# Optimization experiments

Hardware: AMD Instinct MI355X
Metric: run time of the kernel (lower is better)

The kernel has to match this reference:

```python
import jax, jax.numpy as jnp
import numpy as np

C = 3.0              # Poincare ball curvature (hard-coded in module)
SQRT_C = np.float32(np.sqrt(3.0))
MIN_NORM = 1e-15     # geoopt MIN_NORM clamp
EPS = 1e-5           # artanh clamp for fp32
TEMP = 0.07


def setup_inputs() -> dict:
    key = jax.random.key(0)
    ks = jax.random.split(key, 6)
    B, F_IN, H, D, N = 4096, 768, 256, 128, 16384
    x = jax.random.normal(ks[0], (B, F_IN), jnp.float32)
    W1 = jax.random.normal(ks[1], (F_IN, H), jnp.float32) * np.float32(1.0 / np.sqrt(F_IN))
    b1 = jnp.zeros((H,), jnp.float32)
    W2 = jax.random.normal(ks[2], (H, H), jnp.float32) * np.float32(1.0 / np.sqrt(H))
    b2 = jnp.zeros((H,), jnp.float32)
    W3 = jax.random.normal(ks[3], (H, D), jnp.float32) * np.float32(1.0 / np.sqrt(H))
    b3 = jnp.zeros((D,), jnp.float32)
    # prototypes: unit directions scaled by 0.95/c (as in __init__), inside radius 1/sqrt(c)
    g = jax.random.normal(ks[4], (N, D), jnp.float32)
    prototypes = g / jnp.linalg.norm(g, axis=1, keepdims=True) * np.float32(0.95 / C)
    return {"x": x, "W1": W1, "b1": b1, "W2": W2, "b2": b2,
            "W3": W3, "b3": b3, "prototypes": prototypes}


def _expmap0(u):
    # geoopt expmap0: tanh(sqrt(c)*||u||) * u / (sqrt(c)*||u||)
    un = jnp.maximum(jnp.linalg.norm(u, axis=-1, keepdims=True), MIN_NORM)
    return jnp.tanh(SQRT_C * un) * u / (SQRT_C * un)


def _pairwise_poincare_dist(p, h):
    # dist(x,y) = 2/sqrt(c) * artanh( sqrt(c) * || (-x) mobius_add y || )
    # Expanded via dot products so no [B,N,D] intermediate is materialized.
    A = jnp.sum(p * p, axis=-1)            # [N]  ||p||^2
    Bn = jnp.sum(h * h, axis=-1)           # [B]  ||h||^2
    P = h @ p.T                            # [B,N] <h, p>
    # mobius_add(-p, h): <-p, h> = -P
    alpha = 1.0 - 2.0 * C * P + C * Bn[:, None]
    beta = 1.0 - C * A[None, :]
    denom = jnp.maximum(1.0 - 2.0 * C * P + (C * C) * A[None, :] * Bn[:, None], MIN_NORM)
    num_sq = alpha * alpha * A[None, :] + beta * beta * Bn[:, None] - 2.0 * alpha * beta * P
    mnorm = jnp.sqrt(jnp.maximum(num_sq, MIN_NORM)) / denom   # [B,N]
    arg = jnp.minimum(SQRT_C * mnorm, 1.0 - EPS)
    return (2.0 / SQRT_C) * jnp.arctanh(arg)                  # [B,N]


def reference(x, W1, b1, W2, b2, W3, b3, prototypes):
    # Mlp: Linear -> GELU -> Linear -> GELU -> Linear (exact erf GELU, torch default)
    h = jax.nn.gelu(x @ W1 + b1, approximate=False)
    h = jax.nn.gelu(h @ W2 + b2, approximate=False)
    u = h @ W3 + b3                       # [B, D] Euclidean embedding
    hyp = _expmap0(u)                     # [B, D] on Poincare ball
    dist = _pairwise_poincare_dist(prototypes, hyp)  # [B, N]
    logits = -dist / TEMP
    return logits, hyp
```

## Files before the change

kernel.cpp:

```cpp
#include <hip/hip_runtime.h>
#include <math.h>

#define BB 4096
#define FIN 768
#define HH 256
#define DD 128
#define NN 16384

typedef _Float16 half8 __attribute__((ext_vector_type(8)));
typedef _Float16 half4 __attribute__((ext_vector_type(4)));
typedef float floatx4 __attribute__((ext_vector_type(4)));

__global__ void transpose_kernel(const float* __restrict__ in, float* __restrict__ out,
                                 int K, int N) {
  __shared__ float tile[32][33];
  int k0 = blockIdx.y * 32, n0 = blockIdx.x * 32;
  int tx = threadIdx.x, ty = threadIdx.y;
  for (int r = ty; r < 32; r += 8) {
    tile[r][tx] = in[(size_t)(k0 + r) * N + (n0 + tx)];
  }
  __syncthreads();
  for (int r = ty; r < 32; r += 8) {
    out[(size_t)(n0 + r) * K + (k0 + tx)] = tile[tx][r];
  }
}

__global__ void proto_norms(const float* __restrict__ p, float* __restrict__ An) {
  int row = blockIdx.x * 4 + (threadIdx.x >> 6);
  int lane = threadIdx.x & 63;
  float v0 = p[(size_t)row * DD + lane], v1 = p[(size_t)row * DD + 64 + lane];
  float s = v0 * v0 + v1 * v1;
  for (int off = 32; off; off >>= 1) s += __shfl_xor(s, off);
  if (lane == 0) An[row] = s;
}

__global__ void expmap_kernel(const float* __restrict__ u, float* __restrict__ hyp,
                              float* __restrict__ sB) {
  int row = blockIdx.x * 4 + (threadIdx.x >> 6);
  int lane = threadIdx.x & 63;
  float u0 = u[(size_t)row * DD + lane], u1 = u[(size_t)row * DD + 64 + lane];
  double s = (double)u0 * u0 + (double)u1 * u1;
  for (int off = 32; off; off >>= 1) s += __shfl_xor(s, off);
  double un = sqrt(s);
  if (un < 1e-15) un = 1e-15;
  double t = 1.7320508075688772 * un;
  double factor = tanh(t) / t;
  float h0 = (float)(factor * u0), h1 = (float)(factor * u1);
  hyp[(size_t)row * DD + lane] = h0;
  hyp[(size_t)row * DD + 64 + lane] = h1;
  double bs = (double)h0 * h0 + (double)h1 * h1;
  for (int off = 32; off; off >>= 1) bs += __shfl_xor(bs, off);
  if (lane == 0) sB[row] = (float)(1.0 - 3.0 * bs);
}

template <int ACT>
__global__ __launch_bounds__(256) void gemm64(const float* __restrict__ A,
                                              const float* __restrict__ Bt,
                                              const float* __restrict__ bias,
                                              float* __restrict__ C,
                                              int M, int N, int K) {
  __shared__ __align__(16) float As[64 * 128];
  __shared__ __align__(16) float Bs[64 * 128];
  const int tx = threadIdx.x & 15, ty = threadIdx.x >> 4;
  const int brow = blockIdx.x * 64, bcol = blockIdx.y * 64;
  float acc[4][4] = {};
  const int r0 = threadIdx.x >> 5;
  const int c0 = threadIdx.x & 31;

  for (int kb = 0; kb < K; kb += 128) {
#pragma unroll
    for (int s = 0; s < 8; ++s) {
      int r = r0 + 8 * s;
      int sw = ((c0 ^ (r & 31)) << 2);
      *reinterpret_cast<float4*>(&As[r * 128 + sw]) =
          *reinterpret_cast<const float4*>(&A[(size_t)(brow + r) * K + kb + c0 * 4]);
      *reinterpret_cast<float4*>(&Bs[r * 128 + sw]) =
          *reinterpret_cast<const float4*>(&Bt[(size_t)(bcol + r) * K + kb + c0 * 4]);
    }
    __syncthreads();
#pragma unroll
    for (int kk = 0; kk < 32; ++kk) {
      float4 a[4], b[4];
#pragma unroll
      for (int i = 0; i < 4; ++i) {
        int m = ty + 16 * i;
        a[i] = *reinterpret_cast<const float4*>(&As[m * 128 + ((kk ^ (m & 31)) << 2)]);
      }
#pragma unroll
      for (int j = 0; j < 4; ++j) {
        int n = tx + 16 * j;
        b[j] = *reinterpret_cast<const float4*>(&Bs[n * 128 + ((kk ^ (n & 31)) << 2)]);
      }
#pragma unroll
      for (int i = 0; i < 4; ++i)
#pragma unroll
        for (int j = 0; j < 4; ++j) {
          acc[i][j] += a[i].x * b[j].x;
          acc[i][j] += a[i].y * b[j].y;
          acc[i][j] += a[i].z * b[j].z;
          acc[i][j] += a[i].w * b[j].w;
        }
    }
    __syncthreads();
  }
#pragma unroll
  for (int i = 0; i < 4; ++i) {
    int m = brow + ty + 16 * i;
#pragma unroll
    for (int j = 0; j < 4; ++j) {
      int n = bcol + tx + 16 * j;
      float v = acc[i][j] + bias[n];
      if (ACT) v = 0.5f * v * (1.0f + erff(v * 0.70710678f));
      C[(size_t)m * N + n] = v;
    }
  }
}

__global__ __launch_bounds__(256) void dist_mfma(const float* __restrict__ hyp,
                                                 const float* __restrict__ proto,
                                                 const float* __restrict__ An,
                                                 const float* __restrict__ sB,
                                                 float* __restrict__ out) {
  __shared__ __align__(16) char smem[65536];
  const int AHI = 0, ALO = 16384, BHI = 32768, BLO = 49152;

  const int tid = threadIdx.x;
  const int lane = tid & 63;
  const int wave = tid >> 6;
  const int wr = wave >> 1, wc = wave & 1;
  const int l15 = lane & 15, lg = lane >> 4;

  const int brow = blockIdx.y * 128, bcol = blockIdx.x * 128;

  floatx4 acc[4][4] = {};

  const int sr = tid >> 4;
  const int k4 = tid & 15;

  for (int kb = 0; kb < 128; kb += 64) {
#pragma unroll
    for (int s = 0; s < 8; ++s) {
      int row = sr + 16 * s;
      float4 av = *reinterpret_cast<const float4*>(&hyp[(size_t)(brow + row) * DD + kb + k4 * 4]);
      float4 bv = *reinterpret_cast<const float4*>(&proto[(size_t)(bcol + row) * DD + kb + k4 * 4]);
      half4 ahi, alo, bhi, blo;
      ahi[0] = (_Float16)av.x; alo[0] = (_Float16)(av.x - (float)ahi[0]);
      ahi[1] = (_Float16)av.y; alo[1] = (_Float16)(av.y - (float)ahi[1]);
      ahi[2] = (_Float16)av.z; alo[2] = (_Float16)(av.z - (float)ahi[2]);
      ahi[3] = (_Float16)av.w; alo[3] = (_Float16)(av.w - (float)ahi[3]);
      bhi[0] = (_Float16)bv.x; blo[0] = (_Float16)(bv.x - (float)bhi[0]);
      bhi[1] = (_Float16)bv.y; blo[1] = (_Float16)(bv.y - (float)bhi[1]);
      bhi[2] = (_Float16)bv.z; blo[2] = (_Float16)(bv.z - (float)bhi[2]);
      bhi[3] = (_Float16)bv.w; blo[3] = (_Float16)(bv.w - (float)bhi[3]);
      int off = row * 128 + ((k4 * 8) ^ ((row & 7) << 4));
      *reinterpret_cast<half4*>(&smem[AHI + off]) = ahi;
      *reinterpret_cast<half4*>(&smem[ALO + off]) = alo;
      *reinterpret_cast<half4*>(&smem[BHI + off]) = bhi;
      *reinterpret_cast<half4*>(&smem[BLO + off]) = blo;
    }
    __syncthreads();

#pragma unroll
    for (int kkb = 0; kkb < 8; kkb += 4) {
      half8 fahi[4], falo[4], fbhi[4], fblo[4];
      int k8 = kkb + lg;
#pragma unroll
      for (int f = 0; f < 4; ++f) {
        int rA = wr * 64 + f * 16 + l15;
        int offA = rA * 128 + ((k8 << 4) ^ ((rA & 7) << 4));
        fahi[f] = *reinterpret_cast<const half8*>(&smem[AHI + offA]);
        falo[f] = *reinterpret_cast<const half8*>(&smem[ALO + offA]);
        int rB = wc * 64 + f * 16 + l15;
        int offB = rB * 128 + ((k8 << 4) ^ ((rB & 7) << 4));
        fbhi[f] = *reinterpret_cast<const half8*>(&smem[BHI + offB]);
        fblo[f] = *reinterpret_cast<const half8*>(&smem[BLO + offB]);
      }
#pragma unroll
      for (int i = 0; i < 4; ++i)
#pragma unroll
        for (int j = 0; j < 4; ++j) {
          acc[i][j] = __builtin_amdgcn_mfma_f32_16x16x32_f16(fahi[i], fbhi[j], acc[i][j], 0, 0, 0);
          acc[i][j] = __builtin_amdgcn_mfma_f32_16x16x32_f16(fahi[i], fblo[j], acc[i][j], 0, 0, 0);
          acc[i][j] = __builtin_amdgcn_mfma_f32_16x16x32_f16(falo[i], fbhi[j], acc[i][j], 0, 0, 0);
        }
    }
    __syncthreads();
  }

  float aa[4], beta[4], a9[4];
#pragma unroll
  for (int j = 0; j < 4; ++j) {
    aa[j] = An[bcol + wc * 64 + j * 16 + l15];
    beta[j] = 1.0f - 3.0f * aa[j];
    a9[j] = 9.0f * aa[j];
  }
#pragma unroll
  for (int i = 0; i < 4; ++i) {
#pragma unroll
    for (int t = 0; t < 4; ++t) {
      int row = brow + wr * 64 + i * 16 + lg * 4 + t;
      float s = sB[row];
      float bbv = (1.0f - s) * 0.33333334f;
      size_t orow = (size_t)row * NN;
#pragma unroll
      for (int j = 0; j < 4; ++j) {
        float P = acc[i][j][t];
        float t6 = fmaf(-6.0f, P, 1.0f);
        float alpha = fmaf(3.0f, bbv, t6);
        float den = fmaf(a9[j], bbv, t6);
        den = fmaxf(den, 1e-15f);
        float ns = alpha * alpha * aa[j] + beta[j] * beta[j] * bbv
                   - 2.0f * alpha * beta[j] * P;
        ns = fmaxf(ns, 1e-15f);
        float om = beta[j] * s / (den + sqrtf(3.0f * ns));
        om = fmaxf(om, 1e-5f);
        float ratio = __fdividef(2.0f - om, om);
        out[orow + (bcol + wc * 64 + j * 16 + l15)] = -8.247861f * __logf(ratio);
      }
    }
  }
}

extern "C" void kernel_launch(void* const* d_in, const int* in_sizes, int n_in,
                              void* d_out, int out_size, void* d_ws, size_t ws_size,
                              hipStream_t stream) {
  const float* x  = (const float*)d_in[0];
  const float* W1 = (const float*)d_in[1];
  const float* b1 = (const float*)d_in[2];
  const float* W2 = (const float*)d_in[3];
  const float* b2 = (const float*)d_in[4];
  const float* W3 = (const float*)d_in[5];
  const float* b3 = (const float*)d_in[6];
  const float* proto = (const float*)d_in[7];

  float* logits = (float*)d_out;
  float* hyp = logits + (size_t)BB * NN;

  float* ws  = (float*)d_ws;
  float* Wt1 = ws;
  float* Wt2 = Wt1 + 256 * 768;
  float* Wt3 = Wt2 + 256 * 256;
  float* h1  = Wt3 + 128 * 256;
  float* h2  = h1 + (size_t)4096 * 256;
  float* uu  = h2 + (size_t)4096 * 256;
  float* An  = uu + (size_t)4096 * 128;
  float* sB  = An + 16384;

  transpose_kernel<<<dim3(8, 24), dim3(32, 8), 0, stream>>>(W1, Wt1, 768, 256);
  transpose_kernel<<<dim3(8, 8), dim3(32, 8), 0, stream>>>(W2, Wt2, 256, 256);
  transpose_kernel<<<dim3(4, 8), dim3(32, 8), 0, stream>>>(W3, Wt3, 256, 128);
  proto_norms<<<4096, 256, 0, stream>>>(proto, An);

  gemm64<1><<<dim3(64, 4), 256, 0, stream>>>(x, Wt1, b1, h1, 4096, 256, 768);
  gemm64<1><<<dim3(64, 4), 256, 0, stream>>>(h1, Wt2, b2, h2, 4096, 256, 256);
  gemm64<0><<<dim3(64, 2), 256, 0, stream>>>(h2, Wt3, b3, uu, 4096, 128, 256);

  expmap_kernel<<<1024, 256, 0, stream>>>(uu, hyp, sB);

  dist_mfma<<<dim3(128, 32), 256, 0, stream>>>(hyp, proto, An, sB, logits);
}
```

Baseline: 266.6 us.

## Precompute fp16 hi/lo splits in MFMA fragment layout and drop LDS staging

The hyp and prototype tensors are now split into fp16 hi/lo parts once, in prep kernels, and written in an MFMA-fragment-ordered global layout. The distance kernel then loads fragments straight from global memory into registers with double-buffered prefetch, with no shared memory and no barriers. The epilogue is also simplified algebraically (fewer ops, log2 instead of divide-then-log). This removes redundant per-block conversion work and LDS traffic, at the cost of extra prep passes, reused workspace buffers and reliance on L2 for operand reuse.

```diff
diff --git a/kernel.cpp b/kernel.cpp
--- a/kernel.cpp
+++ b/kernel.cpp
@@ -8,7 +8,6 @@
 #define NN 16384
 
 typedef _Float16 half8 __attribute__((ext_vector_type(8)));
-typedef _Float16 half4 __attribute__((ext_vector_type(4)));
 typedef float floatx4 __attribute__((ext_vector_type(4)));
 
 __global__ void transpose_kernel(const float* __restrict__ in, float* __restrict__ out,
@@ -25,20 +24,29 @@
   }
 }
 
-__global__ void proto_norms(const float* __restrict__ p, float* __restrict__ An) {
+__global__ void proto_prep(const float* __restrict__ p, _Float16* __restrict__ BHf,
+                           _Float16* __restrict__ BLf, float* __restrict__ beta) {
   int row = blockIdx.x * 4 + (threadIdx.x >> 6);
-  int lane = threadIdx.x & 63;
-  float v0 = p[(size_t)row * DD + lane], v1 = p[(size_t)row * DD + 64 + lane];
-  float s = v0 * v0 + v1 * v1;
+  int l = threadIdx.x & 63;
+  float v0 = p[(size_t)row * DD + l], v1 = p[(size_t)row * DD + 64 + l];
+  double s = (double)v0 * v0 + (double)v1 * v1;
   for (int off = 32; off; off >>= 1) s += __shfl_xor(s, off);
-  if (lane == 0) An[row] = s;
-}
-
-__global__ void expmap_kernel(const float* __restrict__ u, float* __restrict__ hyp,
-                              float* __restrict__ sB) {
+  if (l == 0) beta[row] = (float)(1.0 - 3.0 * s);
+  _Float16 h0 = (_Float16)v0; _Float16 lo0 = (_Float16)(v0 - (float)h0);
+  _Float16 h1 = (_Float16)v1; _Float16 lo1 = (_Float16)(v1 - (float)h1);
+  int g = row >> 4, lr = row & 15, lg = (l >> 3) & 3, e = l & 7;
+  size_t d0 = (size_t)g * 2048 + (size_t)(((l >> 5)) * 4 + lg) * 128 + lr * 8 + e;
+  size_t d1 = (size_t)g * 2048 + (size_t)((2 + (l >> 5)) * 4 + lg) * 128 + lr * 8 + e;
+  BHf[d0] = h0; BLf[d0] = lo0;
+  BHf[d1] = h1; BLf[d1] = lo1;
+}
+
+__global__ void expmap_prep(const float* __restrict__ u, float* __restrict__ hyp,
+                            _Float16* __restrict__ AHf, _Float16* __restrict__ ALf,
+                            float* __restrict__ sB) {
   int row = blockIdx.x * 4 + (threadIdx.x >> 6);
-  int lane = threadIdx.x & 63;
-  float u0 = u[(size_t)row * DD + lane], u1 = u[(size_t)row * DD + 64 + lane];
+  int l = threadIdx.x & 63;
+  float u0 = u[(size_t)row * DD + l], u1 = u[(size_t)row * DD + 64 + l];
   double s = (double)u0 * u0 + (double)u1 * u1;
   for (int off = 32; off; off >>= 1) s += __shfl_xor(s, off);
   double un = sqrt(s);
@@ -46,11 +54,18 @@
   double t = 1.7320508075688772 * un;
   double factor = tanh(t) / t;
   float h0 = (float)(factor * u0), h1 = (float)(factor * u1);
-  hyp[(size_t)row * DD + lane] = h0;
-  hyp[(size_t)row * DD + 64 + lane] = h1;
+  hyp[(size_t)row * DD + l] = h0;
+  hyp[(size_t)row * DD + 64 + l] = h1;
   double bs = (double)h0 * h0 + (double)h1 * h1;
   for (int off = 32; off; off >>= 1) bs += __shfl_xor(bs, off);
-  if (lane == 0) sB[row] = (float)(1.0 - 3.0 * bs);
+  if (l == 0) sB[row] = (float)(1.0 - 3.0 * bs);
+  _Float16 hh0 = (_Float16)h0; _Float16 lo0 = (_Float16)(h0 - (float)hh0);
+  _Float16 hh1 = (_Float16)h1; _Float16 lo1 = (_Float16)(h1 - (float)hh1);
+  int g = row >> 4, lr = row & 15, lg = (l >> 3) & 3, e = l & 7;
+  size_t d0 = (size_t)g * 2048 + (size_t)(((l >> 5)) * 4 + lg) * 128 + lr * 8 + e;
+  size_t d1 = (size_t)g * 2048 + (size_t)((2 + (l >> 5)) * 4 + lg) * 128 + lr * 8 + e;
+  AHf[d0] = hh0; ALf[d0] = lo0;
+  AHf[d1] = hh1; ALf[d1] = lo1;
 }
 
 template <int ACT>
@@ -116,83 +131,56 @@
   }
 }
 
-__global__ __launch_bounds__(256) void dist_mfma(const float* __restrict__ hyp,
-                                                 const float* __restrict__ proto,
-                                                 const float* __restrict__ An,
-                                                 const float* __restrict__ sB,
-                                                 float* __restrict__ out) {
-  __shared__ __align__(16) char smem[65536];
-  const int AHI = 0, ALO = 16384, BHI = 32768, BLO = 49152;
-
-  const int tid = threadIdx.x;
-  const int lane = tid & 63;
-  const int wave = tid >> 6;
+__global__ __launch_bounds__(256, 2) void dist_mfma(
+    const _Float16* __restrict__ AH, const _Float16* __restrict__ AL,
+    const _Float16* __restrict__ BH, const _Float16* __restrict__ BL,
+    const float* __restrict__ beta, const float* __restrict__ sB,
+    float* __restrict__ out) {
+  const int tid = threadIdx.x, lane = tid & 63, wave = tid >> 6;
   const int wr = wave >> 1, wc = wave & 1;
   const int l15 = lane & 15, lg = lane >> 4;
-
   const int brow = blockIdx.y * 128, bcol = blockIdx.x * 128;
 
+  const size_t aB = (size_t)((brow >> 4) + wr * 4) * 2048 + (size_t)lg * 128 + l15 * 8;
+  const size_t bB = (size_t)((bcol >> 4) + wc * 4) * 2048 + (size_t)lg * 128 + l15 * 8;
+
   floatx4 acc[4][4] = {};
-
-  const int sr = tid >> 4;
-  const int k4 = tid & 15;
-
-  for (int kb = 0; kb < 128; kb += 64) {
-#pragma unroll
-    for (int s = 0; s < 8; ++s) {
-      int row = sr + 16 * s;
-      float4 av = *reinterpret_cast<const float4*>(&hyp[(size_t)(brow + row) * DD + kb + k4 * 4]);
-      float4 bv = *reinterpret_cast<const float4*>(&proto[(size_t)(bcol + row) * DD + kb + k4 * 4]);
-      half4 ahi, alo, bhi, blo;
-      ahi[0] = (_Float16)av.x; alo[0] = (_Float16)(av.x - (float)ahi[0]);
-      ahi[1] = (_Float16)av.y; alo[1] = (_Float16)(av.y - (float)ahi[1]);
-      ahi[2] = (_Float16)av.z; alo[2] = (_Float16)(av.z - (float)ahi[2]);
-      ahi[3] = (_Float16)av.w; alo[3] = (_Float16)(av.w - (float)ahi[3]);
-      bhi[0] = (_Float16)bv.x; blo[0] = (_Float16)(bv.x - (float)bhi[0]);
-      bhi[1] = (_Float16)bv.y; blo[1] = (_Float16)(bv.y - (float)bhi[1]);
-      bhi[2] = (_Float16)bv.z; blo[2] = (_Float16)(bv.z - (float)bhi[2]);
-      bhi[3] = (_Float16)bv.w; blo[3] = (_Float16)(bv.w - (float)bhi[3]);
-      int off = row * 128 + ((k4 * 8) ^ ((row & 7) << 4));
-      *reinterpret_cast<half4*>(&smem[AHI + off]) = ahi;
-      *reinterpret_cast<half4*>(&smem[ALO + off]) = alo;
-      *reinterpret_cast<half4*>(&smem[BHI + off]) = bhi;
-      *reinterpret_cast<half4*>(&smem[BLO + off]) = blo;
-    }
-    __syncthreads();
-
-#pragma unroll
-    for (int kkb = 0; kkb < 8; kkb += 4) {
-      half8 fahi[4], falo[4], fbhi[4], fblo[4];
-      int k8 = kkb + lg;
-#pragma unroll
-      for (int f = 0; f < 4; ++f) {
-        int rA = wr * 64 + f * 16 + l15;
-        int offA = rA * 128 + ((k8 << 4) ^ ((rA & 7) << 4));
-        fahi[f] = *reinterpret_cast<const half8*>(&smem[AHI + offA]);
-        falo[f] = *reinterpret_cast<const half8*>(&smem[ALO + offA]);
-        int rB = wc * 64 + f * 16 + l15;
-        int offB = rB * 128 + ((k8 << 4) ^ ((rB & 7) << 4));
-        fbhi[f] = *reinterpret_cast<const half8*>(&smem[BHI + offB]);
-        fblo[f] = *reinterpret_cast<const half8*>(&smem[BLO + offB]);
-      }
-#pragma unroll
-      for (int i = 0; i < 4; ++i)
-#pragma unroll
-        for (int j = 0; j < 4; ++j) {
-          acc[i][j] = __builtin_amdgcn_mfma_f32_16x16x32_f16(fahi[i], fbhi[j], acc[i][j], 0, 0, 0);
-          acc[i][j] = __builtin_amdgcn_mfma_f32_16x16x32_f16(fahi[i], fblo[j], acc[i][j], 0, 0, 0);
-          acc[i][j] = __builtin_amdgcn_mfma_f32_16x16x32_f16(falo[i], fbhi[j], acc[i][j], 0, 0, 0);
-        }
-    }
-    __syncthreads();
-  }
-
-  float aa[4], beta[4], a9[4];
+  half8 pah[4], pal[4], pbh[4], pbl[4];
+  half8 qah[4], qal[4], qbh[4], qbl[4];
+
+#define LOADF(Dah, Dal, Dbh, Dbl, KS)                                      \
+  _Pragma("unroll") for (int f = 0; f < 4; ++f) {                          \
+    Dah[f] = *(const half8*)&AH[aB + (size_t)f * 2048 + (KS) * 512];       \
+    Dal[f] = *(const half8*)&AL[aB + (size_t)f * 2048 + (KS) * 512];       \
+    Dbh[f] = *(const half8*)&BH[bB + (size_t)f * 2048 + (KS) * 512];       \
+    Dbl[f] = *(const half8*)&BL[bB + (size_t)f * 2048 + (KS) * 512];       \
+  }
+
+#define MSTEP(Sah, Sal, Sbh, Sbl)                                          \
+  _Pragma("unroll") for (int i = 0; i < 4; ++i) {                          \
+    _Pragma("unroll") for (int j = 0; j < 4; ++j) {                        \
+      acc[i][j] = __builtin_amdgcn_mfma_f32_16x16x32_f16(Sah[i], Sbh[j], acc[i][j], 0, 0, 0); \
+      acc[i][j] = __builtin_amdgcn_mfma_f32_16x16x32_f16(Sah[i], Sbl[j], acc[i][j], 0, 0, 0); \
+      acc[i][j] = __builtin_amdgcn_mfma_f32_16x16x32_f16(Sal[i], Sbh[j], acc[i][j], 0, 0, 0); \
+    }                                                                      \
+  }
+
+  LOADF(pah, pal, pbh, pbl, 0)
+  LOADF(qah, qal, qbh, qbl, 1)
+  MSTEP(pah, pal, pbh, pbl)
+  LOADF(pah, pal, pbh, pbl, 2)
+  MSTEP(qah, qal, qbh, qbl)
+  LOADF(qah, qal, qbh, qbl, 3)
+  MSTEP(pah, pal, pbh, pbl)
+  MSTEP(qah, qal, qbh, qbl)
+#undef LOADF
+#undef MSTEP
+
+  float bet[4], a9[4];
 #pragma unroll
   for (int j = 0; j < 4; ++j) {
-    aa[j] = An[bcol + wc * 64 + j * 16 + l15];
-    beta[j] = 1.0f - 3.0f * aa[j];
-    a9[j] = 9.0f * aa[j];
+    bet[j] = beta[bcol + wc * 64 + j * 16 + l15];
+    a9[j] = 3.0f * (1.0f - bet[j]);
   }
 #pragma unroll
   for (int i = 0; i < 4; ++i) {
@@ -200,22 +188,21 @@
     for (int t = 0; t < 4; ++t) {
       int row = brow + wr * 64 + i * 16 + lg * 4 + t;
       float s = sB[row];
-      float bbv = (1.0f - s) * 0.33333334f;
+      float bb = (1.0f - s) * 0.33333334f;
       size_t orow = (size_t)row * NN;
 #pragma unroll
       for (int j = 0; j < 4; ++j) {
         float P = acc[i][j][t];
         float t6 = fmaf(-6.0f, P, 1.0f);
-        float alpha = fmaf(3.0f, bbv, t6);
-        float den = fmaf(a9[j], bbv, t6);
+        float den = fmaf(a9[j], bb, t6);
         den = fmaxf(den, 1e-15f);
-        float ns = alpha * alpha * aa[j] + beta[j] * beta[j] * bbv
-                   - 2.0f * alpha * beta[j] * P;
-        ns = fmaxf(ns, 1e-15f);
-        float om = beta[j] * s / (den + sqrtf(3.0f * ns));
+        float bs = bet[j] * s;
+        float q = den * (den - bs);
+        q = fmaxf(q, 0.0f);
+        float om = __fdividef(bs, den + sqrtf(q));
         om = fmaxf(om, 1e-5f);
-        float ratio = __fdividef(2.0f - om, om);
-        out[orow + (bcol + wc * 64 + j * 16 + l15)] = -8.247861f * __logf(ratio);
+        out[orow + bcol + wc * 64 + j * 16 + l15] =
+            -5.7169818f * (__log2f(2.0f - om) - __log2f(om));
       }
     }
   }
@@ -236,26 +223,30 @@
   float* logits = (float*)d_out;
   float* hyp = logits + (size_t)BB * NN;
 
-  float* ws  = (float*)d_ws;
-  float* Wt1 = ws;
-  float* Wt2 = Wt1 + 256 * 768;
-  float* Wt3 = Wt2 + 256 * 256;
-  float* h1  = Wt3 + 128 * 256;
-  float* h2  = h1 + (size_t)4096 * 256;
-  float* uu  = h2 + (size_t)4096 * 256;
-  float* An  = uu + (size_t)4096 * 128;
-  float* sB  = An + 16384;
+  float* ws   = (float*)d_ws;
+  float* h1   = ws;
+  float* h2   = ws + 1048576;
+  float* uu   = ws + 2097152;
+  float* Wt1  = ws + 2621440;
+  float* Wt2  = ws + 2818048;
+  float* Wt3  = ws + 2883584;
+  float* beta = ws + 2916352;
+  float* sB   = ws + 2932736;
+  _Float16* AHf = (_Float16*)(ws + 2936832);
+  _Float16* ALf = AHf + (size_t)4096 * 128;
+  _Float16* BHf = (_Float16*)h1;
+  _Float16* BLf = (_Float16*)h2;
 
   transpose_kernel<<<dim3(8, 24), dim3(32, 8), 0, stream>>>(W1, Wt1, 768, 256);
   transpose_kernel<<<dim3(8, 8), dim3(32, 8), 0, stream>>>(W2, Wt2, 256, 256);
   transpose_kernel<<<dim3(4, 8), dim3(32, 8), 0, stream>>>(W3, Wt3, 256, 128);
-  proto_norms<<<4096, 256, 0, stream>>>(proto, An);
 
   gemm64<1><<<dim3(64, 4), 256, 0, stream>>>(x, Wt1, b1, h1, 4096, 256, 768);
   gemm64<1><<<dim3(64, 4), 256, 0, stream>>>(h1, Wt2, b2, h2, 4096, 256, 256);
   gemm64<0><<<dim3(64, 2), 256, 0, stream>>>(h2, Wt3, b3, uu, 4096, 128, 256);
 
-  expmap_kernel<<<1024, 256, 0, stream>>>(uu, hyp, sB);
-
-  dist_mfma<<<dim3(128, 32), 256, 0, stream>>>(hyp, proto, An, sB, logits);
-}
+  proto_prep<<<4096, 256, 0, stream>>>(proto, BHf, BLf, beta);
+  expmap_prep<<<1024, 256, 0, stream>>>(uu, hyp, AHf, ALf, sB);
+
+  dist_mfma<<<dim3(128, 32), 256, 0, stream>>>(AHf, ALf, BHf, BLf, beta, sB, logits);
+}
```

Result: faster. 224.2 us (-15.9%).
